# Kernel optimization log

Measured on AMD Instinct MI355X. Metric: run time of the kernel, lower is better.

## Reference

```python
import jax, jax.numpy as jnp
import numpy as np
from jax.scipy.linalg import cho_solve

BLOCKSIZE = 128   # sharded_gptc.BLOCKSIZE
PERC_DAMP = 0.01


def _get_divisible_blocksize(dim: int, blocksize_top: int) -> int:
    b = blocksize_top
    while dim % b != 0:
        b -= 1
    return b


def setup_inputs() -> dict:
    key = jax.random.key(0)
    x = jax.random.normal(key, (4, 2048, 1024), dtype=jnp.float32)
    return {"x": x, "ca": 2}


def reference(x, ca):
    # --- reshape/transpose bookkeeping from GptqHinvCollector.__call__ ---
    ca_axes = (int(ca),)
    transpose = [a for a in range(x.ndim) if a not in ca_axes] + list(ca_axes)
    x = x.transpose(transpose)
    features = int(np.prod(x.shape[-len(ca_axes):]))
    x = x.reshape((-1, features))                      # (rows, F)
    blocksize = _get_divisible_blocksize(x.shape[0], BLOCKSIZE)
    xb = x.reshape((-1, blocksize, features))          # (nblocks, bs, F)

    # --- _init_hinv_for_calibration: damped diagonal initialization ---
    diag = jnp.mean(jnp.float32(xb) ** 2, (0, 1))      # (F,)
    damp = PERC_DAMP * jnp.mean(diag)
    hinv0 = jnp.diag(jnp.ones(features, jnp.float32) / damp)  # (damp*I)^-1

    # --- compute_hinv: blocked Woodbury / Cholesky recursion over row blocks ---
    # hinv_{k+1} = (hinv_k^{-1} + B^T B)^{-1}
    #            = hinv_k - hinv_k B^T (I + B hinv_k B^T)^{-1} B hinv_k
    eye_b = jnp.eye(blocksize, dtype=jnp.float32)

    def block_update(hinv, B):
        HB = hinv @ B.T                                # (F, bs)
        S = eye_b + B @ HB                             # (bs, bs), SPD
        L = jnp.linalg.cholesky(S)
        W = cho_solve((L, True), HB.T)                 # S^{-1} (B hinv): (bs, F)
        return hinv - HB @ W, None

    hinv, _ = jax.lax.scan(block_update, hinv0, xb)

    # act_order=False -> identity permutation
    perm = jnp.arange(features, dtype=jnp.int32)

    # CALIBRATE path after init: collected_hinv = hinv, num_calibrated_batches = 1
    num_calibrated_batches = jnp.int32(1)
    return hinv * num_calibrated_batches, perm
```

## Files before the change

kernel.cpp:

```cpp
#include <hip/hip_runtime.h>
#include <math.h>

#define F 1024
#define NROWS 8192
#define NELEM (NROWS * F)

typedef unsigned short ushort_t;
typedef short bf16x8 __attribute__((ext_vector_type(8)));
typedef float f32x4 __attribute__((ext_vector_type(4)));
typedef unsigned short ushort8 __attribute__((ext_vector_type(8)));

__device__ __forceinline__ ushort_t f2bf(float f) {
  unsigned u = __float_as_uint(f);
  unsigned r = (u + 0x7fffu + ((u >> 16) & 1u)) >> 16;
  return (ushort_t)r;
}
__device__ __forceinline__ float bf2f(ushort_t b) {
  return __uint_as_float(((unsigned)b) << 16);
}

typedef const __attribute__((address_space(1))) unsigned int* gas_ptr;
typedef __attribute__((address_space(3))) unsigned int* las_ptr;
__device__ __forceinline__ void gload16(const void* g, const void* l) {
  __builtin_amdgcn_global_load_lds((gas_ptr)(unsigned long long)g,
                                   (las_ptr)(unsigned int)(unsigned long long)l,
                                   16, 0, 0);
}

__global__ __launch_bounds__(256) void tconv_kernel(const float* __restrict__ x,
                                                    ushort_t* __restrict__ xthi,
                                                    ushort_t* __restrict__ xtlo,
                                                    float* __restrict__ partial) {
    __shared__ ushort_t th[64][68];
    __shared__ ushort_t tl[64][68];
    __shared__ float sdata[256];
    int c0 = blockIdx.x * 64;
    int r0 = blockIdx.y * 64;
    int tid = threadIdx.x;
    float ss = 0.f;
#pragma unroll
    for (int i = 0; i < 4; ++i) {
        int q = tid + 256 * i;
        int r = q >> 4;
        int cq = (q & 15) << 2;
        float4 vx = *(const float4*)&x[(size_t)(r0 + r) * 1024 + c0 + cq];
        float vv[4] = {vx.x, vx.y, vx.z, vx.w};
#pragma unroll
        for (int j = 0; j < 4; ++j) {
            ss = fmaf(vv[j], vv[j], ss);
            ushort_t h = f2bf(vv[j]);
            ushort_t l = f2bf(vv[j] - bf2f(h));
            th[r][cq + j] = h;
            tl[r][cq + j] = l;
        }
    }
    sdata[tid] = ss;
    __syncthreads();
    for (int off = 128; off > 0; off >>= 1) {
        if (tid < off) sdata[tid] += sdata[tid + off];
        __syncthreads();
    }
    if (tid == 0) partial[blockIdx.y * 16 + blockIdx.x] = sdata[0];
#pragma unroll
    for (int i = 0; i < 2; ++i) {
        int q = tid + 256 * i;
        int c = q >> 3;
        int rq = (q & 7) << 3;
        ushort8 oh, ol;
#pragma unroll
        for (int j = 0; j < 8; ++j) {
            oh[j] = th[rq + j][c];
            ol[j] = tl[rq + j][c];
        }
        *(ushort8*)&xthi[(size_t)(c0 + c) * 8192 + r0 + rq] = oh;
        *(ushort8*)&xtlo[(size_t)(c0 + c) * 8192 + r0 + rq] = ol;
    }
}

__device__ __forceinline__ void stage128(const ushort_t* __restrict__ gp, int row0, int kk,
                                         ushort_t* sbase, int w, int lane) {
#pragma unroll
    for (int half = 0; half < 2; ++half) {
        int s = half * 256 + (w << 6) + lane;
        int r = s >> 2, pos = s & 3;
        int kc = (pos ^ ((r >> 1) & 3)) << 3;
        gload16(gp + (size_t)(row0 + r) * 8192 + kk + kc,
                sbase + (size_t)((half << 8) + (w << 6)) * 8);
    }
}

__global__ __launch_bounds__(256, 2) void syrk_mfma_kernel(
    const ushort_t* __restrict__ XThi, const ushort_t* __restrict__ XTlo,
    float* __restrict__ P)
{
    __shared__ ushort_t smem[2][16384];
    int id = blockIdx.x;
    int z = id & 7, t = id >> 3;
    int bi = 0;
    while ((bi + 1) * (bi + 2) / 2 <= t) ++bi;
    int bj = t - bi * (bi + 1) / 2;
    int arow0 = bi * 128, brow0 = bj * 128;
    int k0 = z * 1024;

    int tid = threadIdx.x, lane = tid & 63, w = tid >> 6;
    int wm = w >> 1, wn = w & 1;
    int lr = lane & 15, cg = lane >> 4;

    f32x4 zero4 = {0.f, 0.f, 0.f, 0.f};
    f32x4 acc[4][4];
#pragma unroll
    for (int a = 0; a < 4; ++a)
#pragma unroll
        for (int b = 0; b < 4; ++b) acc[a][b] = zero4;

#define SY_STAGE_F(BUF, KT)                                                        \
    {                                                                              \
        ushort_t* sb = smem[BUF];                                                  \
        int kk = k0 + ((KT) << 5);                                                 \
        stage128(XThi, arow0, kk, sb + 0, w, lane);                                \
        stage128(XTlo, arow0, kk, sb + 4096, w, lane);                             \
        stage128(XThi, brow0, kk, sb + 8192, w, lane);                             \
        stage128(XTlo, brow0, kk, sb + 12288, w, lane);                            \
    }

#define SY_STAGE_D(BUF, KT)                                                        \
    {                                                                              \
        ushort_t* sb = smem[BUF];                                                  \
        int kk = k0 + ((KT) << 5);                                                 \
        stage128(XThi, arow0, kk, sb + 0, w, lane);                                \
        stage128(XTlo, arow0, kk, sb + 4096, w, lane);                             \
    }

#define SY_COMP(BUF, BH, BL)                                                       \
    {                                                                              \
        const ushort_t* sb = smem[BUF];                                            \
        bf16x8 ah[4], bh[4], al[4], bl[4];                                         \
        _Pragma("unroll")                                                          \
        for (int fx = 0; fx < 4; ++fx) {                                           \
            int xo = (cg ^ ((lr >> 1) & 3)) << 3;                                  \
            int ao = ((wm << 6) + (fx << 4) + lr) * 32 + xo;                       \
            int bo = ((wn << 6) + (fx << 4) + lr) * 32 + xo;                       \
            ah[fx] = *(const bf16x8*)&sb[0 + ao];                                  \
            al[fx] = *(const bf16x8*)&sb[4096 + ao];                               \
            bh[fx] = *(const bf16x8*)&sb[(BH) + bo];                               \
            bl[fx] = *(const bf16x8*)&sb[(BL) + bo];                               \
        }                                                                          \
        _Pragma("unroll")                                                          \
        for (int fm = 0; fm < 4; ++fm)                                             \
            _Pragma("unroll")                                                      \
            for (int fn = 0; fn < 4; ++fn) {                                       \
                acc[fm][fn] = __builtin_amdgcn_mfma_f32_16x16x32_bf16(             \
                    ah[fm], bh[fn], acc[fm][fn], 0, 0, 0);                         \
                acc[fm][fn] = __builtin_amdgcn_mfma_f32_16x16x32_bf16(             \
                    ah[fm], bl[fn], acc[fm][fn], 0, 0, 0);                         \
                acc[fm][fn] = __builtin_amdgcn_mfma_f32_16x16x32_bf16(             \
                    al[fm], bh[fn], acc[fm][fn], 0, 0, 0);                         \
            }                                                                      \
    }

    if (bi != bj) {
        SY_STAGE_F(0, 0)
        for (int kt = 0; kt < 31; ++kt) {
            int buf = kt & 1;
            if (buf == 0) SY_STAGE_F(1, kt + 1) else SY_STAGE_F(0, kt + 1)
            asm volatile("s_waitcnt vmcnt(8)" ::: "memory");
            __builtin_amdgcn_s_barrier();
            __builtin_amdgcn_sched_barrier(0);
            if (buf == 0) SY_COMP(0, 8192, 12288) else SY_COMP(1, 8192, 12288)
            __builtin_amdgcn_sched_barrier(0);
            __builtin_amdgcn_s_barrier();
        }
        asm volatile("s_waitcnt vmcnt(0)" ::: "memory");
        __builtin_amdgcn_s_barrier();
        __builtin_amdgcn_sched_barrier(0);
        SY_COMP(1, 8192, 12288)
    } else {
        SY_STAGE_D(0, 0)
        for (int kt = 0; kt < 31; ++kt) {
            int buf = kt & 1;
            if (buf == 0) SY_STAGE_D(1, kt + 1) else SY_STAGE_D(0, kt + 1)
            asm volatile("s_waitcnt vmcnt(4)" ::: "memory");
            __builtin_amdgcn_s_barrier();
            __builtin_amdgcn_sched_barrier(0);
            if (buf == 0) SY_COMP(0, 0, 4096) else SY_COMP(1, 0, 4096)
            __builtin_amdgcn_sched_barrier(0);
            __builtin_amdgcn_s_barrier();
        }
        asm volatile("s_waitcnt vmcnt(0)" ::: "memory");
        __builtin_amdgcn_s_barrier();
        __builtin_amdgcn_sched_barrier(0);
        SY_COMP(1, 0, 4096)
    }

    float* Pt = P + ((size_t)(t * 8 + z) << 14);
#pragma unroll
    for (int fm = 0; fm < 4; ++fm)
#pragma unroll
        for (int fn = 0; fn < 4; ++fn)
#pragma unroll
            for (int rr = 0; rr < 4; ++rr) {
                int row = (wm << 6) + fm * 16 + cg * 4 + rr;
                int col = (wn << 6) + fn * 16 + lr;
                Pt[row * 128 + col] = acc[fm][fn][rr];
            }
}

__global__ void reduceH_kernel(const float* __restrict__ P, const float* __restrict__ part,
                               ushort_t* __restrict__ Hhi, ushort_t* __restrict__ Hlo) {
    __shared__ float red[256];
    int tid = threadIdx.x;
    float s0 = 0.f;
    for (int i = tid; i < 2048; i += 256) s0 += part[i];
    red[tid] = s0;
    __syncthreads();
    for (int off = 128; off > 0; off >>= 1) {
        if (tid < off) red[tid] += red[tid + off];
        __syncthreads();
    }
    float damp = 0.01f * (red[0] / (float)NELEM);

    int b = blockIdx.x;
    int tile = b >> 6;
    int li = ((b & 63) << 8) + tid;
    int bi = 0;
    while ((bi + 1) * (bi + 2) / 2 <= tile) ++bi;
    int bj = tile - bi * (bi + 1) / 2;
    const float* Pt = P + ((size_t)tile << 17);
    float s = 0.f;
#pragma unroll
    for (int z = 0; z < 8; ++z) s += Pt[((size_t)z << 14) + li];
    int r = li >> 7, c = li & 127;
    int gi = bi * 128 + r, gj = bj * 128 + c;
    if (gi == gj) s += damp;
    ushort_t h = f2bf(s), l = f2bf(s - bf2f(h));
    Hhi[gi * F + gj] = h;
    Hlo[gi * F + gj] = l;
    if (bi != bj) {
        Hhi[gj * F + gi] = h;
        Hlo[gj * F + gi] = l;
    }
}

__global__ void matvec_bf16_kernel(const ushort_t* __restrict__ Hhi, const float* __restrict__ v,
                                   float* __restrict__ y, int first) {
    __shared__ float sdata[256];
    int row = blockIdx.x, tid = threadIdx.x;
    float s = 0.f;
    if (first) {
        for (int j = tid; j < F; j += 256) s += bf2f(Hhi[row * F + j]);
    } else {
        for (int j = tid; j < F; j += 256) s = fmaf(bf2f(Hhi[row * F + j]), v[j], s);
    }
    sdata[tid] = s;
    __syncthreads();
    for (int off = 128; off > 0; off >>= 1) {
        if (tid < off) sdata[tid] += sdata[tid + off];
        __syncthreads();
    }
    if (tid == 0) y[row] = sdata[0];
}

__global__ void initX1_kernel(const ushort_t* __restrict__ Hhi, const ushort_t* __restrict__ Hlo,
                              ushort_t* __restrict__ Xhi, ushort_t* __restrict__ Xlo,
                              const float* __restrict__ y, float* __restrict__ scal) {
    __shared__ float red[256];
    int tid = threadIdx.x;
    float4 a = ((const float4*)y)[tid];
    float s = a.x * a.x + a.y * a.y + a.z * a.z + a.w * a.w;
    red[tid] = s;
    __syncthreads();
    for (int off = 128; off > 0; off >>= 1) {
        if (tid < off) red[tid] += red[tid + off];
        __syncthreads();
    }
    float lam = sqrtf(red[0]) * (1.0f / 32.0f);
    float c = 1.0f / (1.15f * lam);
    if (blockIdx.x == 0 && tid == 0) { scal[2] = lam; scal[3] = c; }
    float c2 = c * c;
    int idx0 = (blockIdx.x * 256 + tid) * 4;
#pragma unroll
    for (int k = 0; k < 4; ++k) {
        int idx = idx0 + k;
        float hv = bf2f(Hhi[idx]) + bf2f(Hlo[idx]);
        float val = -c2 * hv + (((idx >> 10) == (idx & 1023)) ? 2.f * c : 0.f);
        ushort_t h = f2bf(val);
        Xhi[idx] = h;
        Xlo[idx] = f2bf(val - bf2f(h));
    }
}

__device__ __forceinline__ void stage64(const ushort_t* __restrict__ gp, int row0, int kk,
                                        ushort_t* sbase, int tid) {
    int r = tid >> 2, pos = tid & 3;
    int kc = (pos ^ ((r >> 1) & 3)) << 3;
    gload16(gp + (size_t)(row0 + r) * 1024 + kk + kc, sbase + (size_t)(tid >> 6 << 9));
}

template <int TERMS, int MODE>
__global__ __launch_bounds__(256) void ns_gemm_kernel(
    const ushort_t* __restrict__ Ahi, const ushort_t* __restrict__ Alo,
    const ushort_t* __restrict__ Bhi, const ushort_t* __restrict__ Blo,
    const ushort_t* __restrict__ Xchi, const ushort_t* __restrict__ Xclo,
    ushort_t* __restrict__ Ohi, ushort_t* __restrict__ Olo,
    float* __restrict__ Of)
{
    constexpr int SLOT = (TERMS == 3) ? 8192 : 4096;
    __shared__ ushort_t smem[4 * SLOT];
    int tid = threadIdx.x, lane = tid & 63, w = tid >> 6;
    int wm = w >> 1, wn = w & 1;
    int row0 = blockIdx.y * 64, col0 = blockIdx.x * 64;
    int lr = lane & 15, cg = lane >> 4;

    f32x4 zero4 = {0.f, 0.f, 0.f, 0.f};
    f32x4 acc[2][2];
#pragma unroll
    for (int a = 0; a < 2; ++a)
#pragma unroll
        for (int b = 0; b < 2; ++b) acc[a][b] = zero4;

#define NS_STAGE(KT)                                                               \
    {                                                                              \
        ushort_t* sb = smem + (size_t)((KT) & 3) * SLOT;                           \
        int kk = (KT) << 5;                                                        \
        stage64(Ahi, row0, kk, sb + 0, tid);                                       \
        stage64(Bhi, col0, kk, sb + 2048, tid);                                    \
        if constexpr (TERMS == 3) {                                                \
            stage64(Alo, row0, kk, sb + 4096, tid);                                \
            stage64(Blo, col0, kk, sb + 6144, tid);                                \
        }                                                                          \
    }

#define NS_COMPUTE(KT)                                                             \
    {                                                                              \
        const ushort_t* sb = smem + (size_t)((KT) & 3) * SLOT;                     \
        bf16x8 ah[2], bh[2], al[2], bl[2];                                         \
        _Pragma("unroll")                                                          \
        for (int fx = 0; fx < 2; ++fx) {                                           \
            int xo = (cg ^ ((lr >> 1) & 3)) << 3;                                  \
            int ao = ((wm << 5) + (fx << 4) + lr) * 32 + xo;                       \
            int bo = ((wn << 5) + (fx << 4) + lr) * 32 + xo;                       \
            ah[fx] = *(const bf16x8*)&sb[0 + ao];                                  \
            bh[fx] = *(const bf16x8*)&sb[2048 + bo];                               \
            if constexpr (TERMS == 3) {                                            \
                al[fx] = *(const bf16x8*)&sb[4096 + ao];                           \
                bl[fx] = *(const bf16x8*)&sb[6144 + bo];                           \
            }                                                                      \
        }                                                                          \
        _Pragma("unroll")                                                          \
        for (int fm = 0; fm < 2; ++fm)                                             \
            _Pragma("unroll")                                                      \
            for (int fn = 0; fn < 2; ++fn) {                                       \
                acc[fm][fn] = __builtin_amdgcn_mfma_f32_16x16x32_bf16(             \
                    ah[fm], bh[fn], acc[fm][fn], 0, 0, 0);                         \
                if constexpr (TERMS == 3) {                                        \
                    acc[fm][fn] = __builtin_amdgcn_mfma_f32_16x16x32_bf16(         \
                        ah[fm], bl[fn], acc[fm][fn], 0, 0, 0);                     \
                    acc[fm][fn] = __builtin_amdgcn_mfma_f32_16x16x32_bf16(         \
                        al[fm], bh[fn], acc[fm][fn], 0, 0, 0);                     \
                }                                                                  \
            }                                                                      \
    }

    NS_STAGE(0)
    NS_STAGE(1)
    for (int kt = 0; kt < 30; ++kt) {
        NS_STAGE(kt + 2)
        if constexpr (TERMS == 3) { asm volatile("s_waitcnt vmcnt(8)" ::: "memory"); }
        else                      { asm volatile("s_waitcnt vmcnt(4)" ::: "memory"); }
        __builtin_amdgcn_s_barrier();
        __builtin_amdgcn_sched_barrier(0);
        NS_COMPUTE(kt)
        __builtin_amdgcn_sched_barrier(0);
    }
    if constexpr (TERMS == 3) { asm volatile("s_waitcnt vmcnt(4)" ::: "memory"); }
    else                      { asm volatile("s_waitcnt vmcnt(2)" ::: "memory"); }
    __builtin_amdgcn_s_barrier();
    __builtin_amdgcn_sched_barrier(0);
    NS_COMPUTE(30)
    asm volatile("s_waitcnt vmcnt(0)" ::: "memory");
    __builtin_amdgcn_s_barrier();
    __builtin_amdgcn_sched_barrier(0);
    NS_COMPUTE(31)

#pragma unroll
    for (int fm = 0; fm < 2; ++fm)
#pragma unroll
        for (int fn = 0; fn < 2; ++fn)
#pragma unroll
            for (int rr = 0; rr < 4; ++rr) {
                int r = row0 + (wm << 5) + fm * 16 + cg * 4 + rr;
                int c = col0 + (wn << 5) + fn * 16 + lr;
                size_t idx = (size_t)r * F + c;
                float val = acc[fm][fn][rr];
                if constexpr (MODE == 0) {
                    ushort_t h = f2bf(val);
                    Ohi[idx] = h;
                    Olo[idx] = f2bf(val - bf2f(h));
                } else {
                    float xc = bf2f(Xchi[idx]) + bf2f(Xclo[idx]);
                    val = 2.0f * xc - val;
                    if constexpr (MODE == 1) {
                        ushort_t h = f2bf(val);
                        Ohi[idx] = h;
                        Olo[idx] = f2bf(val - bf2f(h));
                    } else {
                        Of[idx] = val;
                    }
                }
            }
    if constexpr (MODE == 2) {
        if (blockIdx.x == 0 && blockIdx.y == 0) {
            int i0 = tid * 4;
#pragma unroll
            for (int k = 0; k < 4; ++k)
                Of[(size_t)F * F + i0 + k] = (float)(i0 + k);
        }
    }
}

__global__ void sumsq_partial_kernel(const float* __restrict__ x, float* __restrict__ partial) {
    __shared__ float sdata[256];
    int tid = threadIdx.x;
    int base = blockIdx.x * 4096;
    float s = 0.f;
    for (int i = tid; i < 4096; i += 256) {
        float v = x[base + i];
        s = fmaf(v, v, s);
    }
    sdata[tid] = s;
    __syncthreads();
    for (int off = 128; off > 0; off >>= 1) {
        if (tid < off) sdata[tid] += sdata[tid + off];
        __syncthreads();
    }
    if (tid == 0) partial[blockIdx.x] = sdata[0];
}

__global__ void finish_damp_kernel(const float* __restrict__ partial, float* __restrict__ scal) {
    __shared__ float sdata[256];
    int tid = threadIdx.x;
    float s = 0.f;
    for (int i = tid; i < 2048; i += 256) s += partial[i];
    sdata[tid] = s;
    __syncthreads();
    for (int off = 128; off > 0; off >>= 1) {
        if (tid < off) sdata[tid] += sdata[tid + off];
        __syncthreads();
    }
    if (tid == 0) {
        float mean = sdata[0] / (float)NELEM;
        scal[1] = 0.01f * mean;
    }
}

__global__ void init_v_kernel(float* __restrict__ v) {
    int i = blockIdx.x * 256 + threadIdx.x;
    if (i < F) v[i] = 1.0f;
}

__global__ void matvec_kernel(const float* __restrict__ H, const float* __restrict__ v,
                              float* __restrict__ y) {
    __shared__ float sdata[256];
    int row = blockIdx.x, tid = threadIdx.x;
    float s = 0.f;
    for (int j = tid; j < F; j += 256) s = fmaf(H[row * F + j], v[j], s);
    sdata[tid] = s;
    __syncthreads();
    for (int off = 128; off > 0; off >>= 1) {
        if (tid < off) sdata[tid] += sdata[tid + off];
        __syncthreads();
    }
    if (tid == 0) y[row] = sdata[0];
}

__global__ void normalize_kernel(const float* __restrict__ y, float* __restrict__ v,
                                 float* __restrict__ scal) {
    __shared__ float sdata[256];
    __shared__ float lam;
    int tid = threadIdx.x;
    float s = 0.f;
    for (int i = tid; i < F; i += 256) {
        float t = y[i];
        s = fmaf(t, t, s);
    }
    sdata[tid] = s;
    __syncthreads();
    for (int off = 128; off > 0; off >>= 1) {
        if (tid < off) sdata[tid] += sdata[tid + off];
        __syncthreads();
    }
    if (tid == 0) {
        lam = sqrtf(sdata[0]);
        scal[2] = lam;
        scal[3] = 1.0f / (1.05f * lam);
    }
    __syncthreads();
    float il = 1.0f / lam;
    for (int i = tid; i < F; i += 256) v[i] = y[i] * il;
}

__global__ __launch_bounds__(256) void syrk_kernel(const float* __restrict__ X,
                                                   float* __restrict__ H,
                                                   const float* __restrict__ scal) {
    __shared__ float LA[16][64];
    __shared__ float LB[16][64];
    int tx = threadIdx.x, ty = threadIdx.y;
    int t = ty * 16 + tx;
    int i0 = blockIdx.y * 64, j0 = blockIdx.x * 64;
    int lk = t >> 4;
    int lc = (t & 15) << 2;
    float acc[4][4] = {};
    for (int k0 = 0; k0 < NROWS; k0 += 16) {
        int r = (k0 + lk) * F;
        float4 a4 = *(const float4*)&X[r + i0 + lc];
        float4 b4 = *(const float4*)&X[r + j0 + lc];
        __syncthreads();
        *(float4*)&LA[lk][lc] = a4;
        *(float4*)&LB[lk][lc] = b4;
        __syncthreads();
#pragma unroll
        for (int kk = 0; kk < 16; ++kk) {
            float4 a = *(const float4*)&LA[kk][ty << 2];
            float4 b = *(const float4*)&LB[kk][tx << 2];
            float av[4] = {a.x, a.y, a.z, a.w};
            float bv[4] = {b.x, b.y, b.z, b.w};
#pragma unroll
            for (int rr = 0; rr < 4; ++rr)
#pragma unroll
                for (int cc = 0; cc < 4; ++cc)
                    acc[rr][cc] = fmaf(av[rr], bv[cc], acc[rr][cc]);
        }
    }
    float damp = scal[1];
#pragma unroll
    for (int rr = 0; rr < 4; ++rr) {
        int i = i0 + (ty << 2) + rr;
#pragma unroll
        for (int cc = 0; cc < 4; ++cc) {
            int j = j0 + (tx << 2) + cc;
            float v = acc[rr][cc];
            if (i == j) v += damp;
            H[i * F + j] = v;
        }
    }
}

__global__ void init_X_kernel(float* __restrict__ A, const float* __restrict__ scal) {
    int idx = blockIdx.x * 256 + threadIdx.x;
    int i = idx >> 10, j = idx & (F - 1);
    A[idx] = (i == j) ? scal[3] : 0.0f;
}

__global__ __launch_bounds__(256) void gemm_nn_kernel(const float* __restrict__ A,
                                                      const float* __restrict__ Bm,
                                                      float* __restrict__ C,
                                                      const float* __restrict__ D,
                                                      int mode) {
    __shared__ float LA[16][64];
    __shared__ float LB[16][64];
    int tx = threadIdx.x, ty = threadIdx.y;
    int t = ty * 16 + tx;
    int i0 = blockIdx.y * 64, j0 = blockIdx.x * 64;
    int aii = t >> 2;
    int akq = (t & 3) << 2;
    int bkk = t >> 4;
    int bjq = (t & 15) << 2;
    float acc[4][4] = {};
    for (int k0 = 0; k0 < F; k0 += 16) {
        float4 a4 = *(const float4*)&A[(i0 + aii) * F + k0 + akq];
        float4 b4 = *(const float4*)&Bm[(k0 + bkk) * F + j0 + bjq];
        __syncthreads();
        LA[akq + 0][aii] = a4.x;
        LA[akq + 1][aii] = a4.y;
        LA[akq + 2][aii] = a4.z;
        LA[akq + 3][aii] = a4.w;
        *(float4*)&LB[bkk][bjq] = b4;
        __syncthreads();
#pragma unroll
        for (int kk = 0; kk < 16; ++kk) {
            float4 a = *(const float4*)&LA[kk][ty << 2];
            float4 b = *(const float4*)&LB[kk][tx << 2];
            float av[4] = {a.x, a.y, a.z, a.w};
            float bv[4] = {b.x, b.y, b.z, b.w};
#pragma unroll
            for (int rr = 0; rr < 4; ++rr)
#pragma unroll
                for (int cc = 0; cc < 4; ++cc)
                    acc[rr][cc] = fmaf(av[rr], bv[cc], acc[rr][cc]);
        }
    }
#pragma unroll
    for (int rr = 0; rr < 4; ++rr) {
        int i = i0 + (ty << 2) + rr;
#pragma unroll
        for (int cc = 0; cc < 4; ++cc) {
            int j = j0 + (tx << 2) + cc;
            float v = acc[rr][cc];
            if (mode == 1) v = 2.0f * D[i * F + j] - v;
            C[i * F + j] = v;
        }
    }
}

__global__ void finalize_kernel(const float* __restrict__ A, float* __restrict__ out) {
    int idx = blockIdx.x * 256 + threadIdx.x;
    if (idx < F * F) out[idx] = A[idx];
    else if (idx < F * F + F) out[idx] = (float)(idx - F * F);
}

extern "C" void kernel_launch(void* const* d_in, const int* in_sizes, int n_in,
                              void* d_out, int out_size, void* d_ws, size_t ws_size,
                              hipStream_t stream) {
    const float* x = (const float*)d_in[0];
    float* out = (float*)d_out;

    char* base = (char*)d_ws;
    size_t off = 0;
    auto alloc = [&](size_t bytes) -> char* {
        char* p = base + off;
        off += bytes;
        off = (off + 255) & ~(size_t)255;
        return p;
    };
    float*    scal = (float*)alloc(64 * 4);
    float*    part = (float*)alloc(2048 * 4);
    ushort_t* XThi = (ushort_t*)alloc((size_t)NELEM * 2);
    ushort_t* XTlo = (ushort_t*)alloc((size_t)NELEM * 2);
    ushort_t* Hhi  = (ushort_t*)alloc((size_t)F * F * 2);
    ushort_t* Hlo  = (ushort_t*)alloc((size_t)F * F * 2);
    ushort_t* X0hi = (ushort_t*)alloc((size_t)F * F * 2);
    ushort_t* X0lo = (ushort_t*)alloc((size_t)F * F * 2);
    ushort_t* X1hi = (ushort_t*)alloc((size_t)F * F * 2);
    ushort_t* X1lo = (ushort_t*)alloc((size_t)F * F * 2);
    ushort_t* Shi  = (ushort_t*)alloc((size_t)F * F * 2);
    ushort_t* Slo  = (ushort_t*)alloc((size_t)F * F * 2);
    float*    v    = (float*)alloc(F * 4);
    float*    y    = (float*)alloc(F * 4);
    float*    P    = (float*)alloc((size_t)36 * 8 * 16384 * 4);
    size_t need = off;

    if (ws_size >= need) {
        tconv_kernel<<<dim3(16, 128), 256, 0, stream>>>(x, XThi, XTlo, part);

        syrk_mfma_kernel<<<288, 256, 0, stream>>>(XThi, XTlo, P);
        reduceH_kernel<<<36 * 64, 256, 0, stream>>>(P, part, Hhi, Hlo);

        matvec_bf16_kernel<<<F, 256, 0, stream>>>(Hhi, v, y, 1);

        initX1_kernel<<<1024, 256, 0, stream>>>(Hhi, Hlo, X0hi, X0lo, y, scal);

        ushort_t* xch = X0hi; ushort_t* xcl = X0lo;
        ushort_t* xnh = X1hi; ushort_t* xnl = X1lo;
        dim3 g(16, 16);
        for (int it = 0; it < 4; ++it) {
            bool last = (it == 3);
            if (it < 1) {
                ns_gemm_kernel<1, 0><<<g, 256, 0, stream>>>(xch, xcl, Hhi, Hlo,
                                                            nullptr, nullptr, Shi, Slo, nullptr);
                ns_gemm_kernel<1, 1><<<g, 256, 0, stream>>>(Shi, Slo, xch, xcl,
                                                            xch, xcl, xnh, xnl, nullptr);
            } else {
                ns_gemm_kernel<3, 0><<<g, 256, 0, stream>>>(xch, xcl, Hhi, Hlo,
                                                            nullptr, nullptr, Shi, Slo, nullptr);
                if (last)
                    ns_gemm_kernel<3, 2><<<g, 256, 0, stream>>>(Shi, Slo, xch, xcl,
                                                                xch, xcl, nullptr, nullptr, out);
                else
                    ns_gemm_kernel<3, 1><<<g, 256, 0, stream>>>(Shi, Slo, xch, xcl,
                                                                xch, xcl, xnh, xnl, nullptr);
            }
            ushort_t* th = xch; xch = xnh; xnh = th;
            ushort_t* tl = xcl; xcl = xnl; xnl = tl;
        }
    } else {
        float* ws = (float*)d_ws;
        float* fscal    = ws;
        float* fpartial = ws + 64;
        float* fH  = ws + 4096;
        float* fA  = fH + F * F;
        float* fB  = fA + F * F;
        float* fv  = fB + F * F;
        float* fy  = fv + F;
        float* R = out;

        sumsq_partial_kernel<<<2048, 256, 0, stream>>>(x, fpartial);
        finish_damp_kernel<<<1, 256, 0, stream>>>(fpartial, fscal);

        dim3 grid16(16, 16), blk16(16, 16);
        syrk_kernel<<<grid16, blk16, 0, stream>>>(x, fH, fscal);

        init_v_kernel<<<4, 256, 0, stream>>>(fv);
        for (int it = 0; it < 12; ++it) {
            matvec_kernel<<<F, 256, 0, stream>>>(fH, fv, fy);
            normalize_kernel<<<1, 256, 0, stream>>>(fy, fv, fscal);
        }

        init_X_kernel<<<(F * F) / 256, 256, 0, stream>>>(fA, fscal);
        float* Xc = fA;
        float* Xn = fB;
        for (int it = 0; it < 8; ++it) {
            gemm_nn_kernel<<<grid16, blk16, 0, stream>>>(fH, Xc, R, nullptr, 0);
            gemm_nn_kernel<<<grid16, blk16, 0, stream>>>(Xc, R, Xn, Xc, 1);
            float* tmp = Xc; Xc = Xn; Xn = tmp;
        }

        finalize_kernel<<<(F * F + F + 255) / 256, 256, 0, stream>>>(Xc, out);
    }
}
```

Before: 163.4 us.

## Use 256x256 SYRK tiles with 1024-thread blocks and re-split K across slices

Replaces the 128x128 SYRK tiling (288 blocks of 256 threads, 8 K-slices) with 256x256 output tiles computed by 1024-thread blocks. Off-diagonal tiles use 16 K-slices and diagonal tiles use 8, for 128 blocks in total. The larger tile raises operand reuse per staged LDS byte and cuts redundant global loads of X^T. The reduction kernel is updated for the new partial layout and uses float4 reads. The trade-off is fewer blocks than CUs (128), single-block occupancy with large LDS, and more partial buffers to sum.

Result: slower. 478.1 us (+192.5%).

```diff
diff --git a/kernel.cpp b/kernel.cpp
--- a/kernel.cpp
+++ b/kernel.cpp
@@ -77,34 +77,41 @@
     }
 }
 
-__device__ __forceinline__ void stage128(const ushort_t* __restrict__ gp, int row0, int kk,
-                                         ushort_t* sbase, int w, int lane) {
-#pragma unroll
-    for (int half = 0; half < 2; ++half) {
-        int s = half * 256 + (w << 6) + lane;
-        int r = s >> 2, pos = s & 3;
-        int kc = (pos ^ ((r >> 1) & 3)) << 3;
-        gload16(gp + (size_t)(row0 + r) * 8192 + kk + kc,
-                sbase + (size_t)((half << 8) + (w << 6)) * 8);
-    }
-}
-
-__global__ __launch_bounds__(256, 2) void syrk_mfma_kernel(
+__device__ __forceinline__ void stage256(const ushort_t* __restrict__ gp, int row0, int kk,
+                                         ushort_t* sbase, int tid) {
+    int r = tid >> 2, pos = tid & 3;
+    int kc = (pos ^ ((r >> 1) & 3)) << 3;
+    gload16(gp + (size_t)(row0 + r) * 8192 + kk + kc, sbase + ((tid >> 6) << 9));
+}
+
+__global__ __launch_bounds__(1024, 1) void syrk256_kernel(
     const ushort_t* __restrict__ XThi, const ushort_t* __restrict__ XTlo,
     float* __restrict__ P)
 {
-    __shared__ ushort_t smem[2][16384];
+    __shared__ ushort_t smem[65536];
     int id = blockIdx.x;
-    int z = id & 7, t = id >> 3;
-    int bi = 0;
-    while ((bi + 1) * (bi + 2) / 2 <= t) ++bi;
-    int bj = t - bi * (bi + 1) / 2;
-    int arow0 = bi * 128, brow0 = bj * 128;
-    int k0 = z * 1024;
-
     int tid = threadIdx.x, lane = tid & 63, w = tid >> 6;
-    int wm = w >> 1, wn = w & 1;
+    int wm = w >> 2, wn = w & 3;
     int lr = lane & 15, cg = lane >> 4;
+
+    bool isfull = id < 96;
+    int bi, bj, z, k0, sliceBase;
+    if (isfull) {
+        int f = id >> 4;
+        z = id & 15;
+        bi = 1;
+        while (bi * (bi + 1) / 2 <= f) ++bi;
+        bj = f - bi * (bi - 1) / 2;
+        k0 = z << 9;
+        sliceBase = (f << 4) + z;
+    } else {
+        int d = (id - 96) >> 3;
+        z = (id - 96) & 7;
+        bi = d; bj = d;
+        k0 = z << 10;
+        sliceBase = 96 + (d << 3) + z;
+    }
+    int arow0 = bi << 8, brow0 = bj << 8;
 
     f32x4 zero4 = {0.f, 0.f, 0.f, 0.f};
     f32x4 acc[4][4];
@@ -113,35 +120,35 @@
 #pragma unroll
         for (int b = 0; b < 4; ++b) acc[a][b] = zero4;
 
-#define SY_STAGE_F(BUF, KT)                                                        \
+#define S2_STAGE_F(BUF, KT)                                                        \
     {                                                                              \
-        ushort_t* sb = smem[BUF];                                                  \
+        ushort_t* sb = smem + (BUF) * 32768;                                       \
         int kk = k0 + ((KT) << 5);                                                 \
-        stage128(XThi, arow0, kk, sb + 0, w, lane);                                \
-        stage128(XTlo, arow0, kk, sb + 4096, w, lane);                             \
-        stage128(XThi, brow0, kk, sb + 8192, w, lane);                             \
-        stage128(XTlo, brow0, kk, sb + 12288, w, lane);                            \
-    }
-
-#define SY_STAGE_D(BUF, KT)                                                        \
+        stage256(XThi, arow0, kk, sb + 0, tid);                                    \
+        stage256(XTlo, arow0, kk, sb + 8192, tid);                                 \
+        stage256(XThi, brow0, kk, sb + 16384, tid);                                \
+        stage256(XTlo, brow0, kk, sb + 24576, tid);                                \
+    }
+
+#define S2_STAGE_D(BUF, KT)                                                        \
     {                                                                              \
-        ushort_t* sb = smem[BUF];                                                  \
+        ushort_t* sb = smem + (BUF) * 16384;                                       \
         int kk = k0 + ((KT) << 5);                                                 \
-        stage128(XThi, arow0, kk, sb + 0, w, lane);                                \
-        stage128(XTlo, arow0, kk, sb + 4096, w, lane);                             \
-    }
-
-#define SY_COMP(BUF, BH, BL)                                                       \
+        stage256(XThi, arow0, kk, sb + 0, tid);                                    \
+        stage256(XTlo, arow0, kk, sb + 8192, tid);                                 \
+    }
+
+#define S2_COMP(SB, BH, BL)                                                        \
     {                                                                              \
-        const ushort_t* sb = smem[BUF];                                            \
-        bf16x8 ah[4], bh[4], al[4], bl[4];                                         \
+        const ushort_t* sb = (SB);                                                 \
+        int xo = (cg ^ ((lr >> 1) & 3)) << 3;                                      \
+        bf16x8 ah[4], al[4], bh[4], bl[4];                                         \
         _Pragma("unroll")                                                          \
         for (int fx = 0; fx < 4; ++fx) {                                           \
-            int xo = (cg ^ ((lr >> 1) & 3)) << 3;                                  \
             int ao = ((wm << 6) + (fx << 4) + lr) * 32 + xo;                       \
             int bo = ((wn << 6) + (fx << 4) + lr) * 32 + xo;                       \
             ah[fx] = *(const bf16x8*)&sb[0 + ao];                                  \
-            al[fx] = *(const bf16x8*)&sb[4096 + ao];                               \
+            al[fx] = *(const bf16x8*)&sb[8192 + ao];                               \
             bh[fx] = *(const bf16x8*)&sb[(BH) + bo];                               \
             bl[fx] = *(const bf16x8*)&sb[(BL) + bo];                               \
         }                                                                          \
@@ -158,50 +165,50 @@
             }                                                                      \
     }
 
-    if (bi != bj) {
-        SY_STAGE_F(0, 0)
-        for (int kt = 0; kt < 31; ++kt) {
-            int buf = kt & 1;
-            if (buf == 0) SY_STAGE_F(1, kt + 1) else SY_STAGE_F(0, kt + 1)
-            asm volatile("s_waitcnt vmcnt(8)" ::: "memory");
+    if (isfull) {
+        S2_STAGE_F(0, 0)
+        for (int kt = 0; kt < 15; ++kt) {
+            if ((kt & 1) == 0) S2_STAGE_F(1, kt + 1) else S2_STAGE_F(0, kt + 1)
+            asm volatile("s_waitcnt vmcnt(4)" ::: "memory");
             __builtin_amdgcn_s_barrier();
             __builtin_amdgcn_sched_barrier(0);
-            if (buf == 0) SY_COMP(0, 8192, 12288) else SY_COMP(1, 8192, 12288)
+            if ((kt & 1) == 0) S2_COMP(smem + 0, 16384, 24576)
+            else               S2_COMP(smem + 32768, 16384, 24576)
             __builtin_amdgcn_sched_barrier(0);
             __builtin_amdgcn_s_barrier();
         }
         asm volatile("s_waitcnt vmcnt(0)" ::: "memory");
         __builtin_amdgcn_s_barrier();
         __builtin_amdgcn_sched_barrier(0);
-        SY_COMP(1, 8192, 12288)
+        S2_COMP(smem + 32768, 16384, 24576)
     } else {
-        SY_STAGE_D(0, 0)
+        S2_STAGE_D(0, 0)
         for (int kt = 0; kt < 31; ++kt) {
-            int buf = kt & 1;
-            if (buf == 0) SY_STAGE_D(1, kt + 1) else SY_STAGE_D(0, kt + 1)
-            asm volatile("s_waitcnt vmcnt(4)" ::: "memory");
+            if ((kt & 1) == 0) S2_STAGE_D(1, kt + 1) else S2_STAGE_D(0, kt + 1)
+            asm volatile("s_waitcnt vmcnt(2)" ::: "memory");
             __builtin_amdgcn_s_barrier();
             __builtin_amdgcn_sched_barrier(0);
-            if (buf == 0) SY_COMP(0, 0, 4096) else SY_COMP(1, 0, 4096)
+            if ((kt & 1) == 0) S2_COMP(smem + 0, 0, 8192)
+            else               S2_COMP(smem + 16384, 0, 8192)
             __builtin_amdgcn_sched_barrier(0);
             __builtin_amdgcn_s_barrier();
         }
         asm volatile("s_waitcnt vmcnt(0)" ::: "memory");
         __builtin_amdgcn_s_barrier();
         __builtin_amdgcn_sched_barrier(0);
-        SY_COMP(1, 0, 4096)
-    }
-
-    float* Pt = P + ((size_t)(t * 8 + z) << 14);
+        S2_COMP(smem + 16384, 0, 8192)
+    }
+
+    float* Pt = P + ((size_t)sliceBase << 16);
 #pragma unroll
     for (int fm = 0; fm < 4; ++fm)
 #pragma unroll
         for (int fn = 0; fn < 4; ++fn)
 #pragma unroll
             for (int rr = 0; rr < 4; ++rr) {
-                int row = (wm << 6) + fm * 16 + cg * 4 + rr;
-                int col = (wn << 6) + fn * 16 + lr;
-                Pt[row * 128 + col] = acc[fm][fn][rr];
+                int row = (wm << 6) + (fm << 4) + (cg << 2) + rr;
+                int col = (wn << 6) + (fn << 4) + lr;
+                Pt[row * 256 + col] = acc[fm][fn][rr];
             }
 }
 
@@ -221,23 +228,40 @@
 
     int b = blockIdx.x;
     int tile = b >> 6;
-    int li = ((b & 63) << 8) + tid;
-    int bi = 0;
-    while ((bi + 1) * (bi + 2) / 2 <= tile) ++bi;
-    int bj = tile - bi * (bi + 1) / 2;
-    const float* Pt = P + ((size_t)tile << 17);
-    float s = 0.f;
-#pragma unroll
-    for (int z = 0; z < 8; ++z) s += Pt[((size_t)z << 14) + li];
-    int r = li >> 7, c = li & 127;
-    int gi = bi * 128 + r, gj = bj * 128 + c;
-    if (gi == gj) s += damp;
-    ushort_t h = f2bf(s), l = f2bf(s - bf2f(h));
-    Hhi[gi * F + gj] = h;
-    Hlo[gi * F + gj] = l;
-    if (bi != bj) {
-        Hhi[gj * F + gi] = h;
-        Hlo[gj * F + gi] = l;
+    int li = ((b & 63) << 10) + (tid << 2);
+    int bi, bj, base, nz;
+    if (tile < 6) {
+        int f = tile;
+        bi = 1;
+        while (bi * (bi + 1) / 2 <= f) ++bi;
+        bj = f - bi * (bi - 1) / 2;
+        base = f << 4;  nz = 16;
+    } else {
+        int d = tile - 6;
+        bi = d; bj = d;
+        base = 96 + (d << 3);  nz = 8;
+    }
+    const float* Pt = P + ((size_t)base << 16);
+    float sx = 0.f, sy = 0.f, sz = 0.f, sw = 0.f;
+    for (int zz = 0; zz < nz; ++zz) {
+        float4 p4 = *(const float4*)&Pt[((size_t)zz << 16) + li];
+        sx += p4.x; sy += p4.y; sz += p4.z; sw += p4.w;
+    }
+    int r = li >> 8, c = li & 255;
+    int gi = (bi << 8) + r;
+    float v4[4] = {sx, sy, sz, sw};
+#pragma unroll
+    for (int k = 0; k < 4; ++k) {
+        int gj = (bj << 8) + c + k;
+        float val = v4[k];
+        if (gi == gj) val += damp;
+        ushort_t h = f2bf(val), l = f2bf(val - bf2f(h));
+        Hhi[gi * F + gj] = h;
+        Hlo[gi * F + gj] = l;
+        if (bi != bj) {
+            Hhi[gj * F + gi] = h;
+            Hlo[gj * F + gi] = l;
+        }
     }
 }
 
@@ -636,17 +660,16 @@
     ushort_t* Slo  = (ushort_t*)alloc((size_t)F * F * 2);
     float*    v    = (float*)alloc(F * 4);
     float*    y    = (float*)alloc(F * 4);
-    float*    P    = (float*)alloc((size_t)36 * 8 * 16384 * 4);
+    float*    P    = (float*)alloc((size_t)128 * 65536 * 4);
     size_t need = off;
 
     if (ws_size >= need) {
         tconv_kernel<<<dim3(16, 128), 256, 0, stream>>>(x, XThi, XTlo, part);
 
-        syrk_mfma_kernel<<<288, 256, 0, stream>>>(XThi, XTlo, P);
-        reduceH_kernel<<<36 * 64, 256, 0, stream>>>(P, part, Hhi, Hlo);
+        syrk256_kernel<<<128, 1024, 0, stream>>>(XThi, XTlo, P);
+        reduceH_kernel<<<640, 256, 0, stream>>>(P, part, Hhi, Hlo);
 
         matvec_bf16_kernel<<<F, 256, 0, stream>>>(Hhi, v, y, 1);
-
         initX1_kernel<<<1024, 256, 0, stream>>>(Hhi, Hlo, X0hi, X0lo, y, scal);
 
         ushort_t* xch = X0hi; ushort_t* xcl = X0lo;
```
